# Kernel optimization log

Hardware: AMD Instinct MI355X
Metric: run time of the kernel (lower is better)

Reference implementation:

```python
import jax, jax.numpy as jnp
import numpy as np
from jax import lax

HIDDEN = 256
N_FEATURES = 128
V_DIM = 64
SEQ_LEN = 1024
BATCH = 256
N_TIMESTEPS = 1024
ALPHA_INIT = 0.001


def setup_inputs() -> dict:
    key = jax.random.key(0)
    ks = jax.random.split(key, 6)
    stdv = 1.0 / np.sqrt(HIDDEN)
    u = lambda k, shape: jax.random.uniform(k, shape, jnp.float32, -stdv, stdv)
    x = jax.random.normal(ks[0], (SEQ_LEN, BATCH, N_FEATURES), jnp.float32)
    h = jax.random.normal(ks[1], (BATCH, HIDDEN), jnp.float32)
    W = u(ks[2], (N_FEATURES, HIDDEN))
    b = u(ks[3], (HIDDEN,))
    V = u(ks[4], (V_DIM, HIDDEN))
    V2 = u(ks[5], (HIDDEN, V_DIM))
    alpha = ALPHA_INIT * jnp.ones((1, N_TIMESTEPS), jnp.float32)  # K=1
    return {"x": x, "h": h, "W": W, "b": b, "V": V, "V2": V2, "alpha": alpha, "K": 1}


def reference(x, h, W, b, V, V2, alpha, K):
    # P = U = V2 @ V + I  (infite2 in the original code)
    P = jnp.matmul(V2, V) + jnp.eye(HIDDEN, dtype=W.dtype)
    # precompute input projection for all steps: [S,B,H]
    wx = jnp.einsum('sbf,fh->sbh', x, W) + b
    at = alpha[:, 0]  # self.t is never incremented in forward, so always column 0

    def step(h_prev, wx_t):
        alpha_vec = wx_t + jnp.matmul(h_prev, P)  # new_wx + b + h@U
        oldh = h_prev
        h_cur = h_prev
        for k in range(K):
            a = at[k]
            pre = jnp.matmul(jnp.matmul(h_cur, P) + alpha_vec, P)
            h_cur = a * (jnp.tanh(pre) - oldh) + (1.0 - a) * h_cur
        return h_cur, None

    h_final, _ = lax.scan(step, h, wx)
    return h_final
```

## Files before the change

### kernel.cpp

```cpp
#include <hip/hip_runtime.h>


#define HID   256
#define NF    128
#define SEQ   1024
#define SSTR  264

typedef __bf16 bf16_t;
typedef __bf16 bf16x8 __attribute__((ext_vector_type(8)));
typedef float  f32x4  __attribute__((ext_vector_type(4)));

__device__ __forceinline__ float fast_tanh(float x) {
    float e = __builtin_amdgcn_exp2f(x * 2.8853900817779268f);
    return 1.0f - 2.0f * __builtin_amdgcn_rcpf(e + 1.0f);
}

__global__ void k_P(const float* __restrict__ V2, const float* __restrict__ V,
                    float* __restrict__ P) {
    __shared__ float v2row[64];
    int i = blockIdx.x, j = threadIdx.x;
    if (j < 64) v2row[j] = V2[i * 64 + j];
    __syncthreads();
    float s = (i == j) ? 1.0f : 0.0f;
    #pragma unroll 4
    for (int v = 0; v < 64; ++v) s += v2row[v] * V[v * HID + j];
    P[i * HID + j] = s;
}

__global__ void k_E(const float* __restrict__ P, bf16_t* __restrict__ E) {
    __shared__ float prow[HID];
    int i = blockIdx.x, j = threadIdx.x;
    prow[j] = P[i * HID + j];
    __syncthreads();
    float s = (i == j) ? -1.0f : 0.0f;
    #pragma unroll 4
    for (int k = 0; k < HID; ++k) s += prow[k] * P[k * HID + j];
    E[i * HID + j] = (bf16_t)s;
}

__global__ void k_WP(const float* __restrict__ W, const float* __restrict__ b,
                     const float* __restrict__ P,
                     bf16_t* __restrict__ WP, float* __restrict__ bP) {
    __shared__ float row[HID];
    int i = blockIdx.x, j = threadIdx.x;
    if (i < NF) {
        row[j] = W[i * HID + j];
        __syncthreads();
        float s = 0.f;
        #pragma unroll 4
        for (int k = 0; k < HID; ++k) s += row[k] * P[k * HID + j];
        WP[i * HID + j] = (bf16_t)s;
    } else {
        row[j] = b[j];
        __syncthreads();
        float s = 0.f;
        #pragma unroll 4
        for (int k = 0; k < HID; ++k) s += row[k] * P[k * HID + j];
        bP[j] = s;
    }
}

__global__ __launch_bounds__(256) void k_wxp(const float* __restrict__ x,
                                             const bf16_t* __restrict__ WP,
                                             const float* __restrict__ bP,
                                             bf16_t* __restrict__ wxp) {
    int lane = threadIdx.x & 63, w = threadIdx.x >> 6;
    int quad = lane >> 4, m = lane & 15;
    bf16x8 Bf[4][4];
    float bPv[4];
    #pragma unroll
    for (int c = 0; c < 4; ++c) {
        int col = w * 64 + c * 16 + m;
        bPv[c] = bP[col];
        #pragma unroll
        for (int kt = 0; kt < 4; ++kt) {
            bf16x8 f;
            #pragma unroll
            for (int j = 0; j < 8; ++j)
                f[j] = WP[(kt * 32 + quad * 8 + j) * HID + col];
            Bf[c][kt] = f;
        }
    }
    for (int i = 0; i < 8; ++i) {
        int tile = blockIdx.x * 8 + i;
        int t = tile >> 4, g = tile & 15;
        const float* xp = x + (((t * 256) + g * 16 + m) * NF + quad * 8);
        f32x4 acc[4];
        #pragma unroll
        for (int c = 0; c < 4; ++c) acc[c] = (f32x4){bPv[c], bPv[c], bPv[c], bPv[c]};
        #pragma unroll
        for (int kt = 0; kt < 4; ++kt) {
            f32x4 xa = *(const f32x4*)(xp + kt * 32);
            f32x4 xb = *(const f32x4*)(xp + kt * 32 + 4);
            bf16x8 a;
            #pragma unroll
            for (int j = 0; j < 4; ++j) { a[j] = (bf16_t)xa[j]; a[4 + j] = (bf16_t)xb[j]; }
            #pragma unroll
            for (int c = 0; c < 4; ++c)
                acc[c] = __builtin_amdgcn_mfma_f32_16x16x32_bf16(a, Bf[c][kt], acc[c], 0, 0, 0);
        }
        bf16x8 lo, hi;
        #pragma unroll
        for (int c = 0; c < 2; ++c)
            #pragma unroll
            for (int r = 0; r < 4; ++r) {
                lo[c * 4 + r] = (bf16_t)acc[c][r];
                hi[c * 4 + r] = (bf16_t)acc[2 + c][r];
            }
        long tb = (long)tile * 512;
        *(bf16x8*)(wxp + (tb + (2 * w) * 64 + lane) * 8)     = lo;
        *(bf16x8*)(wxp + (tb + (2 * w + 1) * 64 + lane) * 8) = hi;
    }
}

__global__ __launch_bounds__(512, 2) void k_scan_pre(const float* __restrict__ h_in,
                                                     const float* __restrict__ alpha,
                                                     const int* __restrict__ Kp,
                                                     const bf16_t* __restrict__ E,
                                                     const bf16_t* __restrict__ wxp,
                                                     float* __restrict__ out) {
    __shared__ bf16_t S[2][16 * SSTR];
    int g = blockIdx.x;
    int tid = threadIdx.x;
    int lane = tid & 63, wv = tid >> 6, quad = lane >> 4, m = lane & 15;
    int colbase = wv * 32 + m;

    bf16x8 Ef[16];
    #pragma unroll
    for (int c = 0; c < 2; ++c) {
        int col = colbase + c * 16;
        #pragma unroll
        for (int kt = 0; kt < 8; ++kt) {
            bf16x8 f;
            #pragma unroll
            for (int j = 0; j < 8; ++j)
                f[j] = E[(kt * 32 + quad * 8 + j) * HID + col];
            Ef[c * 8 + kt] = f;
        }
    }

    float hp[8], hc[8], sreg[8];
    #pragma unroll
    for (int c = 0; c < 2; ++c)
        #pragma unroll
        for (int r = 0; r < 4; ++r) {
            int e = c * 4 + r;
            int row = quad * 4 + r, col = colbase + c * 16;
            float v = h_in[(g * 16 + row) * HID + col];
            hp[e] = v; hc[e] = v; sreg[e] = 2.0f * v;
            S[0][row * SSTR + col] = (bf16_t)(2.0f * v);
        }
    float a = alpha[0];
    float one_ma = 1.0f - a;
    int K = Kp[0];
    if (K < 1 || K > 64) K = 1;
    __syncthreads();

    const bf16x8* wptr = (const bf16x8*)wxp;
    int wbase = g * 512 + tid;
    bf16x8 wx = wptr[wbase];

    int p = 0;
    for (int t = 0; t < SEQ; ++t) {
        int tn = (t + 1 < SEQ) ? t + 1 : t;
        bf16x8 wxn = wptr[tn * (16 * 512) + wbase];

        for (int k = 0; k < K; ++k) {
            f32x4 acc[2];
            #pragma unroll
            for (int c = 0; c < 2; ++c)
                #pragma unroll
                for (int r = 0; r < 4; ++r) acc[c][r] = (float)wx[c * 4 + r];
            const bf16_t* sbase = &S[p][m * SSTR];
            #pragma unroll
            for (int kt = 0; kt < 8; ++kt) {
                bf16x8 af = *(const bf16x8*)(sbase + kt * 32 + quad * 8);
                #pragma unroll
                for (int c = 0; c < 2; ++c)
                    acc[c] = __builtin_amdgcn_mfma_f32_16x16x32_bf16(af, Ef[c * 8 + kt], acc[c], 0, 0, 0);
            }
            bool last = (k == K - 1);
            #pragma unroll
            for (int c = 0; c < 2; ++c) {
                int col = colbase + c * 16;
                #pragma unroll
                for (int r = 0; r < 4; ++r) {
                    int e = c * 4 + r;
                    int row = quad * 4 + r;
                    float pre = acc[c][r] + sreg[e];
                    float T = fast_tanh(pre);
                    float hn = a * (T - hp[e]) + one_ma * hc[e];
                    float sn;
                    if (last) { hp[e] = hn; hc[e] = hn; sn = 2.0f * hn; }
                    else      { hc[e] = hn; sn = hn + hp[e]; }
                    sreg[e] = sn;
                    S[p ^ 1][row * SSTR + col] = (bf16_t)sn;
                }
            }
            p ^= 1;
            __syncthreads();
        }
        wx = wxn;
    }

    #pragma unroll
    for (int c = 0; c < 2; ++c)
        #pragma unroll
        for (int r = 0; r < 4; ++r) {
            int row = quad * 4 + r, col = colbase + c * 16;
            out[(g * 16 + row) * HID + col] = hp[c * 4 + r];
        }
}

__global__ __launch_bounds__(256, 1) void k_scan_fused(const float* __restrict__ h_in,
                                                 const float* __restrict__ alpha,
                                                 const int* __restrict__ Kp,
                                                 const bf16_t* __restrict__ E,
                                                 const bf16_t* __restrict__ WP,
                                                 const float* __restrict__ bP,
                                                 const float* __restrict__ x,
                                                 float* __restrict__ out) {
    __shared__ bf16_t S[2][16 * SSTR];
    int g = blockIdx.x;
    int tid = threadIdx.x;
    int lane = tid & 63, w = tid >> 6, quad = lane >> 4, m = lane & 15;
    int colbase = w * 64 + m;
    bf16x8 Ef[32];
    bf16x8 Wf[16];
    float bPv[4];
    #pragma unroll
    for (int c = 0; c < 4; ++c) {
        int col = colbase + c * 16;
        bPv[c] = bP[col];
        #pragma unroll
        for (int kt = 0; kt < 8; ++kt) {
            bf16x8 f;
            #pragma unroll
            for (int j = 0; j < 8; ++j)
                f[j] = E[(kt * 32 + quad * 8 + j) * HID + col];
            Ef[c * 8 + kt] = f;
        }
        #pragma unroll
        for (int kt = 0; kt < 4; ++kt) {
            bf16x8 f;
            #pragma unroll
            for (int j = 0; j < 8; ++j)
                f[j] = WP[(kt * 32 + quad * 8 + j) * HID + col];
            Wf[c * 4 + kt] = f;
        }
    }
    float hp[16], hc[16], sreg[16];
    #pragma unroll
    for (int c = 0; c < 4; ++c)
        #pragma unroll
        for (int r = 0; r < 4; ++r) {
            int e = c * 4 + r;
            int row = quad * 4 + r, col = colbase + c * 16;
            float v = h_in[(g * 16 + row) * HID + col];
            hp[e] = v; hc[e] = v; sreg[e] = 2.0f * v;
            S[0][row * SSTR + col] = (bf16_t)(2.0f * v);
        }
    float a = alpha[0];
    float one_ma = 1.0f - a;
    int K = Kp[0];
    if (K < 1 || K > 64) K = 1;
    __syncthreads();
    const float* xrow = x + ((g * 16 + m) * NF + quad * 8);
    bf16x8 xf[4];
    #pragma unroll
    for (int kt = 0; kt < 4; ++kt) {
        f32x4 xa = *(const f32x4*)(xrow + kt * 32);
        f32x4 xb = *(const f32x4*)(xrow + kt * 32 + 4);
        bf16x8 f;
        #pragma unroll
        for (int j = 0; j < 4; ++j) { f[j] = (bf16_t)xa[j]; f[4 + j] = (bf16_t)xb[j]; }
        xf[kt] = f;
    }
    int p = 0;
    for (int t = 0; t < SEQ; ++t) {
        int tn = (t + 1 < SEQ) ? t + 1 : t;
        const float* xn = xrow + tn * (256 * NF);
        bf16x8 xnf[4];
        #pragma unroll
        for (int kt = 0; kt < 4; ++kt) {
            f32x4 xa = *(const f32x4*)(xn + kt * 32);
            f32x4 xb = *(const f32x4*)(xn + kt * 32 + 4);
            bf16x8 f;
            #pragma unroll
            for (int j = 0; j < 4; ++j) { f[j] = (bf16_t)xa[j]; f[4 + j] = (bf16_t)xb[j]; }
            xnf[kt] = f;
        }
        f32x4 wxacc[4];
        #pragma unroll
        for (int c = 0; c < 4; ++c) wxacc[c] = (f32x4){bPv[c], bPv[c], bPv[c], bPv[c]};
        #pragma unroll
        for (int kt = 0; kt < 4; ++kt)
            #pragma unroll
            for (int c = 0; c < 4; ++c)
                wxacc[c] = __builtin_amdgcn_mfma_f32_16x16x32_bf16(xf[kt], Wf[c * 4 + kt], wxacc[c], 0, 0, 0);
        for (int k = 0; k < K; ++k) {
            f32x4 acc[4];
            #pragma unroll
            for (int c = 0; c < 4; ++c) acc[c] = wxacc[c];
            const bf16_t* sbase = &S[p][m * SSTR];
            #pragma unroll
            for (int kt = 0; kt < 8; ++kt) {
                bf16x8 af = *(const bf16x8*)(sbase + kt * 32 + quad * 8);
                #pragma unroll
                for (int c = 0; c < 4; ++c)
                    acc[c] = __builtin_amdgcn_mfma_f32_16x16x32_bf16(af, Ef[c * 8 + kt], acc[c], 0, 0, 0);
            }
            bool last = (k == K - 1);
            #pragma unroll
            for (int c = 0; c < 4; ++c) {
                int col = colbase + c * 16;
                #pragma unroll
                for (int r = 0; r < 4; ++r) {
                    int e = c * 4 + r;
                    int row = quad * 4 + r;
                    float pre = acc[c][r] + sreg[e];
                    float T = fast_tanh(pre);
                    float hn = a * (T - hp[e]) + one_ma * hc[e];
                    float sn;
                    if (last) { hp[e] = hn; hc[e] = hn; sn = 2.0f * hn; }
                    else      { hc[e] = hn; sn = hn + hp[e]; }
                    sreg[e] = sn;
                    S[p ^ 1][row * SSTR + col] = (bf16_t)sn;
                }
            }
            p ^= 1;
            __syncthreads();
        }
        #pragma unroll
        for (int kt = 0; kt < 4; ++kt) xf[kt] = xnf[kt];
    }
    #pragma unroll
    for (int c = 0; c < 4; ++c)
        #pragma unroll
        for (int r = 0; r < 4; ++r) {
            int row = quad * 4 + r, col = colbase + c * 16;
            out[(g * 16 + row) * HID + col] = hp[c * 4 + r];
        }
}

extern "C" void kernel_launch(void* const* d_in, const int* in_sizes, int n_in,
                              void* d_out, int out_size, void* d_ws, size_t ws_size,
                              hipStream_t stream) {
    const float* x     = (const float*)d_in[0];
    const float* h     = (const float*)d_in[1];
    const float* W     = (const float*)d_in[2];
    const float* b     = (const float*)d_in[3];
    const float* V     = (const float*)d_in[4];
    const float* V2    = (const float*)d_in[5];
    const float* alpha = (const float*)d_in[6];
    const int*   Kp    = (const int*)d_in[7];

    char* ws = (char*)d_ws;
    float*  P   = (float*)ws;
    bf16_t* E   = (bf16_t*)(ws + (256u << 10));
    bf16_t* WP  = (bf16_t*)(ws + (384u << 10));
    float*  bP  = (float*)(ws + (448u << 10));
    bf16_t* wxp = (bf16_t*)(ws + (512u << 10));
    size_t need = (512u << 10) + (size_t)SEQ * 16 * 512 * 8 * sizeof(bf16_t);

    hipLaunchKernelGGL(k_P,  dim3(256), dim3(256), 0, stream, V2, V, P);
    hipLaunchKernelGGL(k_E,  dim3(256), dim3(256), 0, stream, P, E);
    hipLaunchKernelGGL(k_WP, dim3(129), dim3(256), 0, stream, W, b, P, WP, bP);
    if (ws_size >= need) {
        hipLaunchKernelGGL(k_wxp, dim3(2048), dim3(256), 0, stream, x, WP, bP, wxp);
        hipLaunchKernelGGL(k_scan_pre, dim3(16), dim3(512), 0, stream, h, alpha, Kp, E, wxp, (float*)d_out);
    } else {
        hipLaunchKernelGGL(k_scan_fused, dim3(16), dim3(256), 0, stream, h, alpha, Kp, E, WP, bP, x, (float*)d_out);
    }
}
```

Measured before the change: 1.156 ms.

## Restructure scan kernel: 4 waves, transposed weights, swizzled LDS, K=1 fast path

The scan kernel moves from 8 waves of 512 threads to 4 waves of 256 threads, with each wave covering 64 columns and holding 32 E fragments in registers. E and WP are now stored transposed so fragments load as vector reads instead of strided scalar gathers. The shared-memory state buffer gets an XOR swizzle to reduce bank conflicts. A specialised K==1 path folds the update into a single fma recurrence on q=2h and unrolls two steps at a time. The aim is to shorten the serial per-step critical path and cut barrier cost, at the price of higher register pressure and fewer waves to hide latency.

```diff
diff --git a/kernel.cpp b/kernel.cpp
--- a/kernel.cpp
+++ b/kernel.cpp
@@ -13,6 +13,10 @@
 __device__ __forceinline__ float fast_tanh(float x) {
     float e = __builtin_amdgcn_exp2f(x * 2.8853900817779268f);
     return 1.0f - 2.0f * __builtin_amdgcn_rcpf(e + 1.0f);
+}
+
+__device__ __forceinline__ int s_swz(int row) {
+    return (((row >> 2) ^ (row >> 3)) & 1) << 5;
 }
 
 __global__ void k_P(const float* __restrict__ V2, const float* __restrict__ V,
@@ -27,7 +31,7 @@
     P[i * HID + j] = s;
 }
 
-__global__ void k_E(const float* __restrict__ P, bf16_t* __restrict__ E) {
+__global__ void k_E(const float* __restrict__ P, bf16_t* __restrict__ Et) {
     __shared__ float prow[HID];
     int i = blockIdx.x, j = threadIdx.x;
     prow[j] = P[i * HID + j];
@@ -35,12 +39,12 @@
     float s = (i == j) ? -1.0f : 0.0f;
     #pragma unroll 4
     for (int k = 0; k < HID; ++k) s += prow[k] * P[k * HID + j];
-    E[i * HID + j] = (bf16_t)s;
+    Et[(size_t)j * HID + i] = (bf16_t)s;
 }
 
 __global__ void k_WP(const float* __restrict__ W, const float* __restrict__ b,
                      const float* __restrict__ P,
-                     bf16_t* __restrict__ WP, float* __restrict__ bP) {
+                     bf16_t* __restrict__ WPt, float* __restrict__ bP) {
     __shared__ float row[HID];
     int i = blockIdx.x, j = threadIdx.x;
     if (i < NF) {
@@ -49,7 +53,7 @@
         float s = 0.f;
         #pragma unroll 4
         for (int k = 0; k < HID; ++k) s += row[k] * P[k * HID + j];
-        WP[i * HID + j] = (bf16_t)s;
+        WPt[(size_t)j * NF + i] = (bf16_t)s;
     } else {
         row[j] = b[j];
         __syncthreads();
@@ -61,10 +65,11 @@
 }
 
 __global__ __launch_bounds__(256) void k_wxp(const float* __restrict__ x,
-                                             const bf16_t* __restrict__ WP,
+                                             const bf16_t* __restrict__ WPt,
                                              const float* __restrict__ bP,
                                              bf16_t* __restrict__ wxp) {
-    int lane = threadIdx.x & 63, w = threadIdx.x >> 6;
+    int tid = threadIdx.x;
+    int lane = tid & 63, w = tid >> 6;
     int quad = lane >> 4, m = lane & 15;
     bf16x8 Bf[4][4];
     float bPv[4];
@@ -72,19 +77,15 @@
     for (int c = 0; c < 4; ++c) {
         int col = w * 64 + c * 16 + m;
         bPv[c] = bP[col];
-        #pragma unroll
-        for (int kt = 0; kt < 4; ++kt) {
-            bf16x8 f;
-            #pragma unroll
-            for (int j = 0; j < 8; ++j)
-                f[j] = WP[(kt * 32 + quad * 8 + j) * HID + col];
-            Bf[c][kt] = f;
-        }
+        const bf16_t* wp = WPt + (size_t)col * NF + quad * 8;
+        #pragma unroll
+        for (int kt = 0; kt < 4; ++kt)
+            Bf[c][kt] = *(const bf16x8*)(wp + kt * 32);
     }
     for (int i = 0; i < 8; ++i) {
         int tile = blockIdx.x * 8 + i;
         int t = tile >> 4, g = tile & 15;
-        const float* xp = x + (((t * 256) + g * 16 + m) * NF + quad * 8);
+        const float* xp = x + (((size_t)t * 256 + g * 16 + m) * NF + quad * 8);
         f32x4 acc[4];
         #pragma unroll
         for (int c = 0; c < 4; ++c) acc[c] = (f32x4){bPv[c], bPv[c], bPv[c], bPv[c]};
@@ -92,12 +93,12 @@
         for (int kt = 0; kt < 4; ++kt) {
             f32x4 xa = *(const f32x4*)(xp + kt * 32);
             f32x4 xb = *(const f32x4*)(xp + kt * 32 + 4);
-            bf16x8 a;
-            #pragma unroll
-            for (int j = 0; j < 4; ++j) { a[j] = (bf16_t)xa[j]; a[4 + j] = (bf16_t)xb[j]; }
+            bf16x8 aa;
+            #pragma unroll
+            for (int j = 0; j < 4; ++j) { aa[j] = (bf16_t)xa[j]; aa[4 + j] = (bf16_t)xb[j]; }
             #pragma unroll
             for (int c = 0; c < 4; ++c)
-                acc[c] = __builtin_amdgcn_mfma_f32_16x16x32_bf16(a, Bf[c][kt], acc[c], 0, 0, 0);
+                acc[c] = __builtin_amdgcn_mfma_f32_16x16x32_bf16(aa, Bf[c][kt], acc[c], 0, 0, 0);
         }
         bf16x8 lo, hi;
         #pragma unroll
@@ -107,41 +108,207 @@
                 lo[c * 4 + r] = (bf16_t)acc[c][r];
                 hi[c * 4 + r] = (bf16_t)acc[2 + c][r];
             }
-        long tb = (long)tile * 512;
-        *(bf16x8*)(wxp + (tb + (2 * w) * 64 + lane) * 8)     = lo;
-        *(bf16x8*)(wxp + (tb + (2 * w + 1) * 64 + lane) * 8) = hi;
-    }
-}
-
-__global__ __launch_bounds__(512, 2) void k_scan_pre(const float* __restrict__ h_in,
+        size_t tb = (size_t)tile * 4096;
+        *(bf16x8*)(wxp + tb + tid * 8)        = lo;
+        *(bf16x8*)(wxp + tb + 2048 + tid * 8) = hi;
+    }
+}
+
+__global__ __launch_bounds__(256, 1) void k_scan_pre(const float* __restrict__ h_in,
                                                      const float* __restrict__ alpha,
                                                      const int* __restrict__ Kp,
-                                                     const bf16_t* __restrict__ E,
+                                                     const bf16_t* __restrict__ Et,
                                                      const bf16_t* __restrict__ wxp,
                                                      float* __restrict__ out) {
     __shared__ bf16_t S[2][16 * SSTR];
     int g = blockIdx.x;
     int tid = threadIdx.x;
-    int lane = tid & 63, wv = tid >> 6, quad = lane >> 4, m = lane & 15;
-    int colbase = wv * 32 + m;
-
-    bf16x8 Ef[16];
-    #pragma unroll
-    for (int c = 0; c < 2; ++c) {
+    int lane = tid & 63, w = tid >> 6, quad = lane >> 4, m = lane & 15;
+    int colbase = w * 64 + m;
+
+    bf16x8 Ef[32];
+    #pragma unroll
+    for (int c = 0; c < 4; ++c) {
+        const bf16_t* ep = Et + (size_t)(colbase + c * 16) * HID + quad * 8;
+        #pragma unroll
+        for (int kt = 0; kt < 8; ++kt)
+            Ef[c * 8 + kt] = *(const bf16x8*)(ep + kt * 32);
+    }
+
+    const int rd_base = (m * (SSTR * 2) + quad * 16) ^ s_swz(m);
+    int woff[16];
+    #pragma unroll
+    for (int c = 0; c < 4; ++c)
+        #pragma unroll
+        for (int r = 0; r < 4; ++r) {
+            int row = quad * 4 + r, col = colbase + c * 16;
+            woff[c * 4 + r] = ((row * SSTR + col) * 2) ^ s_swz(row);
+        }
+
+    float a = alpha[0];
+    int K = Kp[0];
+    if (K < 1 || K > 64) K = 1;
+
+    float hv[16];
+    #pragma unroll
+    for (int c = 0; c < 4; ++c)
+        #pragma unroll
+        for (int r = 0; r < 4; ++r) {
+            int e = c * 4 + r;
+            int row = quad * 4 + r, col = colbase + c * 16;
+            float v = h_in[(g * 16 + row) * HID + col];
+            hv[e] = v;
+            *(bf16_t*)((char*)&S[0][0] + woff[e]) = (bf16_t)(2.0f * v);
+        }
+    __syncthreads();
+
+    const bf16_t* wlo = wxp + (size_t)g * 4096 + (size_t)tid * 8;
+    const bf16_t* whi = wlo + 2048;
+    const long WSTR = 65536;
+
+    bf16x8 wl = *(const bf16x8*)wlo;
+    bf16x8 wh = *(const bf16x8*)whi;
+
+    if (K == 1) {
+        const float A2 = 2.0f * a, B2 = 1.0f - 2.0f * a;
+        float q[16];
+        #pragma unroll
+        for (int e = 0; e < 16; ++e) q[e] = 2.0f * hv[e];
+
+        auto step = [&](int p, int t) {
+            int tn = (t + 1 < SEQ) ? t + 1 : t;
+            bf16x8 wln = *(const bf16x8*)(wlo + (long)tn * WSTR);
+            bf16x8 whn = *(const bf16x8*)(whi + (long)tn * WSTR);
+            f32x4 acc[4];
+            #pragma unroll
+            for (int r = 0; r < 4; ++r) {
+                acc[0][r] = (float)wl[r];
+                acc[1][r] = (float)wl[4 + r];
+                acc[2][r] = (float)wh[r];
+                acc[3][r] = (float)wh[4 + r];
+            }
+            const char* sb = (const char*)&S[p][0];
+            #pragma unroll
+            for (int kt = 0; kt < 8; ++kt) {
+                bf16x8 af = *(const bf16x8*)(sb + rd_base + kt * 64);
+                #pragma unroll
+                for (int c = 0; c < 4; ++c)
+                    acc[c] = __builtin_amdgcn_mfma_f32_16x16x32_bf16(af, Ef[c * 8 + kt], acc[c], 0, 0, 0);
+            }
+            char* swp = (char*)&S[p ^ 1][0];
+            #pragma unroll
+            for (int c = 0; c < 4; ++c)
+                #pragma unroll
+                for (int r = 0; r < 4; ++r) {
+                    int e = c * 4 + r;
+                    float pre = acc[c][r] + q[e];
+                    float T = fast_tanh(pre);
+                    float qn = fmaf(A2, T, B2 * q[e]);
+                    q[e] = qn;
+                    *(bf16_t*)(swp + woff[e]) = (bf16_t)qn;
+                }
+            __syncthreads();
+            wl = wln; wh = whn;
+        };
+        for (int t = 0; t < SEQ; t += 2) { step(0, t); step(1, t + 1); }
+
+        #pragma unroll
+        for (int c = 0; c < 4; ++c)
+            #pragma unroll
+            for (int r = 0; r < 4; ++r) {
+                int row = quad * 4 + r, col = colbase + c * 16;
+                out[(g * 16 + row) * HID + col] = 0.5f * q[c * 4 + r];
+            }
+    } else {
+        float hp[16], hc[16], sreg[16];
+        #pragma unroll
+        for (int e = 0; e < 16; ++e) { hp[e] = hv[e]; hc[e] = hv[e]; sreg[e] = 2.0f * hv[e]; }
+        float one_ma = 1.0f - a;
+        int p = 0;
+        for (int t = 0; t < SEQ; ++t) {
+            int tn = (t + 1 < SEQ) ? t + 1 : t;
+            bf16x8 wln = *(const bf16x8*)(wlo + (long)tn * WSTR);
+            bf16x8 whn = *(const bf16x8*)(whi + (long)tn * WSTR);
+            for (int k = 0; k < K; ++k) {
+                f32x4 acc[4];
+                #pragma unroll
+                for (int r = 0; r < 4; ++r) {
+                    acc[0][r] = (float)wl[r];
+                    acc[1][r] = (float)wl[4 + r];
+                    acc[2][r] = (float)wh[r];
+                    acc[3][r] = (float)wh[4 + r];
+                }
+                const char* sb = (const char*)&S[p][0];
+                #pragma unroll
+                for (int kt = 0; kt < 8; ++kt) {
+                    bf16x8 af = *(const bf16x8*)(sb + rd_base + kt * 64);
+                    #pragma unroll
+                    for (int c = 0; c < 4; ++c)
+                        acc[c] = __builtin_amdgcn_mfma_f32_16x16x32_bf16(af, Ef[c * 8 + kt], acc[c], 0, 0, 0);
+                }
+                bool last = (k == K - 1);
+                char* swp = (char*)&S[p ^ 1][0];
+                #pragma unroll
+                for (int c = 0; c < 4; ++c)
+                    #pragma unroll
+                    for (int r = 0; r < 4; ++r) {
+                        int e = c * 4 + r;
+                        float pre = acc[c][r] + sreg[e];
+                        float T = fast_tanh(pre);
+                        float hn = a * (T - hp[e]) + one_ma * hc[e];
+                        float sn;
+                        if (last) { hp[e] = hn; hc[e] = hn; sn = 2.0f * hn; }
+                        else      { hc[e] = hn; sn = hn + hp[e]; }
+                        sreg[e] = sn;
+                        *(bf16_t*)(swp + woff[e]) = (bf16_t)sn;
+                    }
+                p ^= 1;
+                __syncthreads();
+            }
+            wl = wln; wh = whn;
+        }
+        #pragma unroll
+        for (int c = 0; c < 4; ++c)
+            #pragma unroll
+            for (int r = 0; r < 4; ++r) {
+                int row = quad * 4 + r, col = colbase + c * 16;
+                out[(g * 16 + row) * HID + col] = hp[c * 4 + r];
+            }
+    }
+}
+
+__global__ __launch_bounds__(256, 1) void k_scan_fused(const float* __restrict__ h_in,
+                                                 const float* __restrict__ alpha,
+                                                 const int* __restrict__ Kp,
+                                                 const bf16_t* __restrict__ Et,
+                                                 const bf16_t* __restrict__ WPt,
+                                                 const float* __restrict__ bP,
+                                                 const float* __restrict__ x,
+                                                 float* __restrict__ out) {
+    __shared__ bf16_t S[2][16 * SSTR];
+    int g = blockIdx.x;
+    int tid = threadIdx.x;
+    int lane = tid & 63, w = tid >> 6, quad = lane >> 4, m = lane & 15;
+    int colbase = w * 64 + m;
+    bf16x8 Ef[32];
+    bf16x8 Wf[16];
+    float bPv[4];
+    #pragma unroll
+    for (int c = 0; c < 4; ++c) {
         int col = colbase + c * 16;
-        #pragma unroll
-        for (int kt = 0; kt < 8; ++kt) {
-            bf16x8 f;
-            #pragma unroll
-            for (int j = 0; j < 8; ++j)
-                f[j] = E[(kt * 32 + quad * 8 + j) * HID + col];
-            Ef[c * 8 + kt] = f;
-        }
-    }
-
-    float hp[8], hc[8], sreg[8];
-    #pragma unroll
-    for (int c = 0; c < 2; ++c)
+        bPv[c] = bP[col];
+        const bf16_t* ep = Et + (size_t)col * HID + quad * 8;
+        #pragma unroll
+        for (int kt = 0; kt < 8; ++kt)
+            Ef[c * 8 + kt] = *(const bf16x8*)(ep + kt * 32);
+        const bf16_t* wpp = WPt + (size_t)col * NF + quad * 8;
+        #pragma unroll
+        for (int kt = 0; kt < 4; ++kt)
+            Wf[c * 4 + kt] = *(const bf16x8*)(wpp + kt * 32);
+    }
+    float hp[16], hc[16], sreg[16];
+    #pragma unroll
+    for (int c = 0; c < 4; ++c)
         #pragma unroll
         for (int r = 0; r < 4; ++r) {
             int e = c * 4 + r;
@@ -155,33 +322,54 @@
     int K = Kp[0];
     if (K < 1 || K > 64) K = 1;
     __syncthreads();
-
-    const bf16x8* wptr = (const bf16x8*)wxp;
-    int wbase = g * 512 + tid;
-    bf16x8 wx = wptr[wbase];
-
+    const float* xrow = x + ((g * 16 + m) * NF + quad * 8);
+    bf16x8 xf[4];
+    #pragma unroll
+    for (int kt = 0; kt < 4; ++kt) {
+        f32x4 xa = *(const f32x4*)(xrow + kt * 32);
+        f32x4 xb = *(const f32x4*)(xrow + kt * 32 + 4);
+        bf16x8 f;
+        #pragma unroll
+        for (int j = 0; j < 4; ++j) { f[j] = (bf16_t)xa[j]; f[4 + j] = (bf16_t)xb[j]; }
+        xf[kt] = f;
+    }
     int p = 0;
     for (int t = 0; t < SEQ; ++t) {
         int tn = (t + 1 < SEQ) ? t + 1 : t;
-        bf16x8 wxn = wptr[tn * (16 * 512) + wbase];
-
+        const float* xn = xrow + (size_t)tn * (256 * NF);
+        bf16x8 xnf[4];
+        #pragma unroll
+        for (int kt = 0; kt < 4; ++kt) {
+            f32x4 xa = *(const f32x4*)(xn + kt * 32);
+            f32x4 xb = *(const f32x4*)(xn + kt * 32 + 4);
+            bf16x8 f;
+            #pragma unroll
+            for (int j = 0; j < 4; ++j) { f[j] = (bf16_t)xa[j]; f[4 + j] = (bf16_t)xb[j]; }
+            xnf[kt] = f;
+        }
+        f32x4 wxacc[4];
+        #pragma unroll
+        for (int c = 0; c < 4; ++c) wxacc[c] = (f32x4){bPv[c], bPv[c], bPv[c], bPv[c]};
+        #pragma unroll
+        for (int kt = 0; kt < 4; ++kt)
+            #pragma unroll
+            for (int c = 0; c < 4; ++c)
+                wxacc[c] = __builtin_amdgcn_mfma_f32_16x16x32_bf16(xf[kt], Wf[c * 4 + kt], wxacc[c], 0, 0, 0);
         for (int k = 0; k < K; ++k) {
-            f32x4 acc[2];
-            #pragma unroll
-            for (int c = 0; c < 2; ++c)
-                #pragma unroll
-                for (int r = 0; r < 4; ++r) acc[c][r] = (float)wx[c * 4 + r];
+            f32x4 acc[4];
+            #pragma unroll
+            for (int c = 0; c < 4; ++c) acc[c] = wxacc[c];
             const bf16_t* sbase = &S[p][m * SSTR];
             #pragma unroll
             for (int kt = 0; kt < 8; ++kt) {
                 bf16x8 af = *(const bf16x8*)(sbase + kt * 32 + quad * 8);
                 #pragma unroll
-                for (int c = 0; c < 2; ++c)
+                for (int c = 0; c < 4; ++c)
                     acc[c] = __builtin_amdgcn_mfma_f32_16x16x32_bf16(af, Ef[c * 8 + kt], acc[c], 0, 0, 0);
             }
             bool last = (k == K - 1);
             #pragma unroll
-            for (int c = 0; c < 2; ++c) {
+            for (int c = 0; c < 4; ++c) {
                 int col = colbase + c * 16;
                 #pragma unroll
                 for (int r = 0; r < 4; ++r) {
@@ -200,137 +388,6 @@
             p ^= 1;
             __syncthreads();
         }
-        wx = wxn;
-    }
-
-    #pragma unroll
-    for (int c = 0; c < 2; ++c)
-        #pragma unroll
-        for (int r = 0; r < 4; ++r) {
-            int row = quad * 4 + r, col = colbase + c * 16;
-            out[(g * 16 + row) * HID + col] = hp[c * 4 + r];
-        }
-}
-
-__global__ __launch_bounds__(256, 1) void k_scan_fused(const float* __restrict__ h_in,
-                                                 const float* __restrict__ alpha,
-                                                 const int* __restrict__ Kp,
-                                                 const bf16_t* __restrict__ E,
-                                                 const bf16_t* __restrict__ WP,
-                                                 const float* __restrict__ bP,
-                                                 const float* __restrict__ x,
-                                                 float* __restrict__ out) {
-    __shared__ bf16_t S[2][16 * SSTR];
-    int g = blockIdx.x;
-    int tid = threadIdx.x;
-    int lane = tid & 63, w = tid >> 6, quad = lane >> 4, m = lane & 15;
-    int colbase = w * 64 + m;
-    bf16x8 Ef[32];
-    bf16x8 Wf[16];
-    float bPv[4];
-    #pragma unroll
-    for (int c = 0; c < 4; ++c) {
-        int col = colbase + c * 16;
-        bPv[c] = bP[col];
-        #pragma unroll
-        for (int kt = 0; kt < 8; ++kt) {
-            bf16x8 f;
-            #pragma unroll
-            for (int j = 0; j < 8; ++j)
-                f[j] = E[(kt * 32 + quad * 8 + j) * HID + col];
-            Ef[c * 8 + kt] = f;
-        }
-        #pragma unroll
-        for (int kt = 0; kt < 4; ++kt) {
-            bf16x8 f;
-            #pragma unroll
-            for (int j = 0; j < 8; ++j)
-                f[j] = WP[(kt * 32 + quad * 8 + j) * HID + col];
-            Wf[c * 4 + kt] = f;
-        }
-    }
-    float hp[16], hc[16], sreg[16];
-    #pragma unroll
-    for (int c = 0; c < 4; ++c)
-        #pragma unroll
-        for (int r = 0; r < 4; ++r) {
-            int e = c * 4 + r;
-            int row = quad * 4 + r, col = colbase + c * 16;
-            float v = h_in[(g * 16 + row) * HID + col];
-            hp[e] = v; hc[e] = v; sreg[e] = 2.0f * v;
-            S[0][row * SSTR + col] = (bf16_t)(2.0f * v);
-        }
-    float a = alpha[0];
-    float one_ma = 1.0f - a;
-    int K = Kp[0];
-    if (K < 1 || K > 64) K = 1;
-    __syncthreads();
-    const float* xrow = x + ((g * 16 + m) * NF + quad * 8);
-    bf16x8 xf[4];
-    #pragma unroll
-    for (int kt = 0; kt < 4; ++kt) {
-        f32x4 xa = *(const f32x4*)(xrow + kt * 32);
-        f32x4 xb = *(const f32x4*)(xrow + kt * 32 + 4);
-        bf16x8 f;
-        #pragma unroll
-        for (int j = 0; j < 4; ++j) { f[j] = (bf16_t)xa[j]; f[4 + j] = (bf16_t)xb[j]; }
-        xf[kt] = f;
-    }
-    int p = 0;
-    for (int t = 0; t < SEQ; ++t) {
-        int tn = (t + 1 < SEQ) ? t + 1 : t;
-        const float* xn = xrow + tn * (256 * NF);
-        bf16x8 xnf[4];
-        #pragma unroll
-        for (int kt = 0; kt < 4; ++kt) {
-            f32x4 xa = *(const f32x4*)(xn + kt * 32);
-            f32x4 xb = *(const f32x4*)(xn + kt * 32 + 4);
-            bf16x8 f;
-            #pragma unroll
-            for (int j = 0; j < 4; ++j) { f[j] = (bf16_t)xa[j]; f[4 + j] = (bf16_t)xb[j]; }
-            xnf[kt] = f;
-        }
-        f32x4 wxacc[4];
-        #pragma unroll
-        for (int c = 0; c < 4; ++c) wxacc[c] = (f32x4){bPv[c], bPv[c], bPv[c], bPv[c]};
-        #pragma unroll
-        for (int kt = 0; kt < 4; ++kt)
-            #pragma unroll
-            for (int c = 0; c < 4; ++c)
-                wxacc[c] = __builtin_amdgcn_mfma_f32_16x16x32_bf16(xf[kt], Wf[c * 4 + kt], wxacc[c], 0, 0, 0);
-        for (int k = 0; k < K; ++k) {
-            f32x4 acc[4];
-            #pragma unroll
-            for (int c = 0; c < 4; ++c) acc[c] = wxacc[c];
-            const bf16_t* sbase = &S[p][m * SSTR];
-            #pragma unroll
-            for (int kt = 0; kt < 8; ++kt) {
-                bf16x8 af = *(const bf16x8*)(sbase + kt * 32 + quad * 8);
-                #pragma unroll
-                for (int c = 0; c < 4; ++c)
-                    acc[c] = __builtin_amdgcn_mfma_f32_16x16x32_bf16(af, Ef[c * 8 + kt], acc[c], 0, 0, 0);
-            }
-            bool last = (k == K - 1);
-            #pragma unroll
-            for (int c = 0; c < 4; ++c) {
-                int col = colbase + c * 16;
-                #pragma unroll
-                for (int r = 0; r < 4; ++r) {
-                    int e = c * 4 + r;
-                    int row = quad * 4 + r;
-                    float pre = acc[c][r] + sreg[e];
-                    float T = fast_tanh(pre);
-                    float hn = a * (T - hp[e]) + one_ma * hc[e];
-                    float sn;
-                    if (last) { hp[e] = hn; hc[e] = hn; sn = 2.0f * hn; }
-                    else      { hc[e] = hn; sn = hn + hp[e]; }
-                    sreg[e] = sn;
-                    S[p ^ 1][row * SSTR + col] = (bf16_t)sn;
-                }
-            }
-            p ^= 1;
-            __syncthreads();
-        }
         #pragma unroll
         for (int kt = 0; kt < 4; ++kt) xf[kt] = xnf[kt];
     }
@@ -357,19 +414,19 @@
 
     char* ws = (char*)d_ws;
     float*  P   = (float*)ws;
-    bf16_t* E   = (bf16_t*)(ws + (256u << 10));
-    bf16_t* WP  = (bf16_t*)(ws + (384u << 10));
+    bf16_t* Et  = (bf16_t*)(ws + (256u << 10));
+    bf16_t* WPt = (bf16_t*)(ws + (384u << 10));
     float*  bP  = (float*)(ws + (448u << 10));
     bf16_t* wxp = (bf16_t*)(ws + (512u << 10));
     size_t need = (512u << 10) + (size_t)SEQ * 16 * 512 * 8 * sizeof(bf16_t);
 
     hipLaunchKernelGGL(k_P,  dim3(256), dim3(256), 0, stream, V2, V, P);
-    hipLaunchKernelGGL(k_E,  dim3(256), dim3(256), 0, stream, P, E);
-    hipLaunchKernelGGL(k_WP, dim3(129), dim3(256), 0, stream, W, b, P, WP, bP);
+    hipLaunchKernelGGL(k_E,  dim3(256), dim3(256), 0, stream, P, Et);
+    hipLaunchKernelGGL(k_WP, dim3(129), dim3(256), 0, stream, W, b, P, WPt, bP);
     if (ws_size >= need) {
-        hipLaunchKernelGGL(k_wxp, dim3(2048), dim3(256), 0, stream, x, WP, bP, wxp);
-        hipLaunchKernelGGL(k_scan_pre, dim3(16), dim3(512), 0, stream, h, alpha, Kp, E, wxp, (float*)d_out);
+        hipLaunchKernelGGL(k_wxp, dim3(2048), dim3(256), 0, stream, x, WPt, bP, wxp);
+        hipLaunchKernelGGL(k_scan_pre, dim3(16), dim3(256), 0, stream, h, alpha, Kp, Et, wxp, (float*)d_out);
     } else {
-        hipLaunchKernelGGL(k_scan_fused, dim3(16), dim3(256), 0, stream, h, alpha, Kp, E, WP, bP, x, (float*)d_out);
-    }
-}
+        hipLaunchKernelGGL(k_scan_fused, dim3(16), dim3(256), 0, stream, h, alpha, Kp, Et, WPt, bP, x, (float*)d_out);
+    }
+}
```

Result: no change. 1.154 ms (-0.2%).
